# Kernel optimization log

Measured on AMD Instinct MI355X. Metric: run time of the kernel, lower is better.

Reference implementation:

```python
import jax, jax.numpy as jnp
import numpy as np

DIM = 1024
HEADS = 16
HEAD_DIM = DIM // HEADS
LAYERS = 8
HIDDEN = 4 * DIM
VOCAB = 266
MAX_POS = 32768
B = 4
L = 2048
SCALE = HEAD_DIM ** -0.5
EPS = 1e-5


def layer_norm(x, g, b):
    m = jnp.mean(x, axis=-1, keepdims=True)
    v = jnp.mean(jnp.square(x - m), axis=-1, keepdims=True)
    return (x - m) * jax.lax.rsqrt(v + EPS) * g + b


def setup_inputs() -> dict:
    key = jax.random.key(0)
    ks = jax.random.split(key, 16)
    s = 0.02
    return {
        "tokens": jax.random.randint(ks[0], (B, L), 0, VOCAB),
        "tok_emb": jax.random.normal(ks[1], (VOCAB, DIM), jnp.float32) * s,
        "pos_emb": jax.random.normal(ks[2], (MAX_POS, DIM), jnp.float32) * s,
        "ln1_g": jnp.ones((LAYERS, DIM), jnp.float32),
        "ln1_b": jnp.zeros((LAYERS, DIM), jnp.float32),
        "q_w": jax.random.normal(ks[3], (LAYERS, DIM, DIM), jnp.float32) * s,
        "k_w": jax.random.normal(ks[4], (LAYERS, DIM, DIM), jnp.float32) * s,
        "v_w": jax.random.normal(ks[5], (LAYERS, DIM, DIM), jnp.float32) * s,
        "o_w": jax.random.normal(ks[6], (LAYERS, DIM, DIM), jnp.float32) * s,
        "ln2_g": jnp.ones((LAYERS, DIM), jnp.float32),
        "ln2_b": jnp.zeros((LAYERS, DIM), jnp.float32),
        "w1_w": jax.random.normal(ks[7], (LAYERS, HIDDEN, DIM), jnp.float32) * s,
        "wg_w": jax.random.normal(ks[8], (LAYERS, HIDDEN, DIM), jnp.float32) * s,
        "w2_w": jax.random.normal(ks[9], (LAYERS, DIM, HIDDEN), jnp.float32) * s,
        "lnf_g": jnp.ones((DIM,), jnp.float32),
        "lnf_b": jnp.zeros((DIM,), jnp.float32),
        "lm_w": jax.random.normal(ks[10], (VOCAB, DIM), jnp.float32) * s,
    }


def reference(tokens, tok_emb, pos_emb, ln1_g, ln1_b, q_w, k_w, v_w, o_w,
              ln2_g, ln2_b, w1_w, wg_w, w2_w, lnf_g, lnf_b, lm_w):
    Bv, Lv = tokens.shape
    x = tok_emb[tokens] + pos_emb[jnp.arange(Lv)][None, :, :]  # [B,L,D]
    # strictly-upper-triangular causal mask (True = masked)
    rows = jnp.arange(Lv)
    mask = rows[None, :] > rows[:, None]  # [L,L], col > row
    pos_bias = jnp.arange(Lv, dtype=x.dtype) * 0.01  # [L]
    neg_inf = jnp.array(-jnp.inf, dtype=x.dtype)

    for i in range(LAYERS):
        h = layer_norm(x, ln1_g[i], ln1_b[i])
        q = jnp.einsum('bld,ed->ble', h, q_w[i]).reshape(Bv, Lv, HEADS, HEAD_DIM).transpose(0, 2, 1, 3)
        k = jnp.einsum('bld,ed->ble', h, k_w[i]).reshape(Bv, Lv, HEADS, HEAD_DIM).transpose(0, 2, 1, 3)
        v = jnp.einsum('bld,ed->ble', h, v_w[i]).reshape(Bv, Lv, HEADS, HEAD_DIM).transpose(0, 2, 1, 3)
        attn = jnp.einsum('bhqd,bhkd->bhqk', q, k) * SCALE
        attn = jnp.where(mask[None, None, :, :], neg_inf, attn)
        attn = attn + pos_bias[None, None, None, :]
        attn = jax.nn.softmax(attn, axis=-1)
        out = jnp.einsum('bhqk,bhkd->bhqd', attn, v).transpose(0, 2, 1, 3).reshape(Bv, Lv, DIM)
        attn_out = jnp.einsum('bld,ed->ble', out, o_w[i])
        x = x + attn_out
        h2 = layer_norm(x, ln2_g[i], ln2_b[i])
        ff = jnp.einsum('blh,dh->bld', jax.nn.silu(jnp.einsum('bld,hd->blh', h2, w1_w[i])) * jnp.einsum('bld,hd->blh', h2, wg_w[i]), w2_w[i])
        x = x + ff

    last = layer_norm(x[:, -1, :], lnf_g, lnf_b)  # [B, D]
    return jnp.einsum('bd,vd->bv', last, lm_w)  # [B, VOCAB]
```

## Files before the change

kernel.cpp:

```cpp
#include <hip/hip_runtime.h>
#include <hip/hip_bf16.h>
#include <math.h>

#define DIMD 1024
#define HEADS 16
#define HD 64
#define LAYERS 8
#define HIDDEN 4096
#define VOCAB 266
#define NB 4
#define SEQ 2048
#define ROWS (NB*SEQ)
#define LOG2E 1.4426950408889634f
#define QSCALE (0.125f * LOG2E)
#define BIAS2 (0.01f * LOG2E)
#define THR2 8.0f

typedef float f32x4 __attribute__((ext_vector_type(4)));
typedef __bf16 bf16x8 __attribute__((ext_vector_type(8)));
typedef __bf16 bf16x4 __attribute__((ext_vector_type(4)));

__device__ __forceinline__ f32x4 mfma16(bf16x8 a, bf16x8 b, f32x4 c) {
    return __builtin_amdgcn_mfma_f32_16x16x32_bf16(a, b, c, 0, 0, 0);
}

__device__ __forceinline__ void gload16(const __bf16* g, __bf16* l) {
    __builtin_amdgcn_global_load_lds(
        (const __attribute__((address_space(1))) void*)g,
        (__attribute__((address_space(3))) void*)l, 16, 0, 0);
}

__global__ void embed_kernel(const int* __restrict__ tok, const float* __restrict__ te,
                             const float* __restrict__ pe, float* __restrict__ x) {
    int row = blockIdx.x;
    int t = tok[row];
    int l = row & (SEQ - 1);
    int c = threadIdx.x;
    f32x4 tv = *(const f32x4*)(te + (size_t)t * DIMD + c * 4);
    f32x4 pv = *(const f32x4*)(pe + (size_t)l * DIMD + c * 4);
    *(f32x4*)(x + (size_t)row * DIMD + c * 4) = tv + pv;
}

__global__ void cvt_kernel(const float* q, const float* k, const float* v, const float* o,
                           const float* w1, const float* wg, const float* w2,
                           __bf16* __restrict__ dst) {
    const size_t MM = 1024 * 1024;
    const float* src; size_t n; size_t off; int ilv = 0;
    switch (blockIdx.y) {
        case 0: src = q;  n = MM;     off = 0;       break;
        case 1: src = k;  n = MM;     off = MM;      break;
        case 2: src = v;  n = MM;     off = 2 * MM;  break;
        case 3: src = o;  n = MM;     off = 3 * MM;  break;
        case 4: src = w1; n = 4 * MM; off = 4 * MM;  ilv = 1; break;
        case 5: src = wg; n = 4 * MM; off = 4 * MM;  ilv = 2; break;
        default: src = w2; n = 4 * MM; off = 12 * MM; break;
    }
    size_t stride = (size_t)gridDim.x * blockDim.x * 8;
    for (size_t i = ((size_t)blockIdx.x * blockDim.x + threadIdx.x) * 8; i < n; i += stride) {
        f32x4 a = *(const f32x4*)(src + i);
        f32x4 b = *(const f32x4*)(src + i + 4);
        bf16x8 ov;
        ov[0] = (__bf16)a[0]; ov[1] = (__bf16)a[1]; ov[2] = (__bf16)a[2]; ov[3] = (__bf16)a[3];
        ov[4] = (__bf16)b[0]; ov[5] = (__bf16)b[1]; ov[6] = (__bf16)b[2]; ov[7] = (__bf16)b[3];
        size_t di;
        if (ilv) {
            size_t row = i >> 10, col = i & 1023;
            di = off + (((row << 1) | (ilv - 1)) << 10) + col;
        } else {
            di = off + i;
        }
        *(bf16x8*)(dst + di) = ov;
    }
}

template<bool F32OUT>
__global__ void ln_kernel(const float* __restrict__ xin, size_t row_stride,
                          const float* __restrict__ g, const float* __restrict__ bb,
                          void* __restrict__ out) {
    int row = blockIdx.x;
    int c = threadIdx.x;
    const float* xr = xin + (size_t)row * row_stride;
    f32x4 v = *(const f32x4*)(xr + c * 4);
    float s = v[0] + v[1] + v[2] + v[3];
    float s2 = v[0]*v[0] + v[1]*v[1] + v[2]*v[2] + v[3]*v[3];
    #pragma unroll
    for (int o = 32; o; o >>= 1) { s += __shfl_xor(s, o); s2 += __shfl_xor(s2, o); }
    __shared__ float red[8];
    int w = c >> 6, lane = c & 63;
    if (lane == 0) { red[w] = s; red[4 + w] = s2; }
    __syncthreads();
    s = red[0] + red[1] + red[2] + red[3];
    s2 = red[4] + red[5] + red[6] + red[7];
    float mean = s * (1.f / DIMD);
    float var = s2 * (1.f / DIMD) - mean * mean;
    float rstd = rsqrtf(var + 1e-5f);
    f32x4 gv = *(const f32x4*)(g + c * 4);
    f32x4 bv = *(const f32x4*)(bb + c * 4);
    f32x4 o4;
    #pragma unroll
    for (int j = 0; j < 4; ++j) o4[j] = (v[j] - mean) * rstd * gv[j] + bv[j];
    if (F32OUT) {
        *(f32x4*)((float*)out + (size_t)row * DIMD + c * 4) = o4;
    } else {
        bf16x4 hv;
        #pragma unroll
        for (int j = 0; j < 4; ++j) hv[j] = (__bf16)o4[j];
        *(bf16x4*)((__bf16*)out + (size_t)row * DIMD + c * 4) = hv;
    }
}

template<int EPI>
__global__ __launch_bounds__(256, 2)
void gemm_bt(const __bf16* __restrict__ A, const __bf16* __restrict__ W,
             int M, int N, int K,
             __bf16* bdst, float* fdst, float scale) {
    __shared__ __bf16 As[128 * 64];
    __shared__ __bf16 Bs[128 * 64];
    int tid = threadIdx.x;
    int lane = tid & 63, w = tid >> 6;
    int wm = w >> 1, wn = w & 1;
    int g16 = lane >> 4, l16 = lane & 15;
    int m0 = blockIdx.y * 128, n0 = blockIdx.x * 128;
    f32x4 acc[4][4] = {};
    int trow = tid >> 3, tcol = (tid & 7) * 8;
    const __bf16* ga = A + (size_t)(m0 + trow) * K + tcol;
    const __bf16* gb = W + (size_t)(n0 + trow) * K + tcol;

    for (int k0 = 0; k0 < K; k0 += 64) {
        #pragma unroll
        for (int p = 0; p < 4; ++p) {
            gload16(ga + (size_t)(p * 32) * K + k0, As + (p * 256 + w * 64) * 8);
            gload16(gb + (size_t)(p * 32) * K + k0, Bs + (p * 256 + w * 64) * 8);
        }
        __syncthreads();
        #pragma unroll
        for (int kk = 0; kk < 2; ++kk) {
            bf16x8 af[4], bfv[4];
            #pragma unroll
            for (int f = 0; f < 4; ++f) {
                af[f]  = *(const bf16x8*)(As + (wm * 64 + f * 16 + l16) * 64 + kk * 32 + g16 * 8);
                bfv[f] = *(const bf16x8*)(Bs + (wn * 64 + f * 16 + l16) * 64 + kk * 32 + g16 * 8);
            }
            #pragma unroll
            for (int fm = 0; fm < 4; ++fm)
                #pragma unroll
                for (int fn = 0; fn < 4; ++fn)
                    acc[fm][fn] = mfma16(af[fm], bfv[fn], acc[fm][fn]);
        }
        __syncthreads();
    }

    #pragma unroll
    for (int fm = 0; fm < 4; ++fm) {
        int rbase = m0 + wm * 64 + fm * 16 + g16 * 4;
        #pragma unroll
        for (int fn = 0; fn < 4; ++fn) {
            int col = n0 + wn * 64 + fn * 16 + l16;
            if (EPI == 2) {
                #pragma unroll
                for (int j = 0; j < 4; ++j) {
                    size_t idx = (size_t)(rbase + j) * N + col;
                    fdst[idx] += acc[fm][fn][j];
                }
            } else if (EPI == 5) {
                int which = col >> 10;
                int c = col & 1023;
                int hh = c >> 6, d = c & 63;
                if (which == 2) {
                    int b = rbase >> 11, l = rbase & 2047;
                    __bf16* vp = bdst + 2 * (size_t)ROWS * DIMD;
                    bf16x4 hv;
                    #pragma unroll
                    for (int j = 0; j < 4; ++j) hv[j] = (__bf16)acc[fm][fn][j];
                    *(bf16x4*)(vp + ((size_t)(b * HEADS + hh) * HD + d) * SEQ + l) = hv;
                } else {
                    float sc = (which == 0) ? scale : 1.f;
                    __bf16* base = bdst + (size_t)which * ROWS * DIMD;
                    #pragma unroll
                    for (int j = 0; j < 4; ++j) {
                        int row = rbase + j;
                        int b = row >> 11, l = row & 2047;
                        base[(((size_t)(b * HEADS + hh) * SEQ + l) << 6) + d] =
                            (__bf16)(acc[fm][fn][j] * sc);
                    }
                }
            } else if (EPI == 6) {
                #pragma unroll
                for (int j = 0; j < 4; ++j) {
                    float own = acc[fm][fn][j];
                    float other = __shfl_xor(own, 1);
                    if (!(l16 & 1)) {
                        float si = own / (1.f + __expf(-own));
                        bdst[(size_t)(rbase + j) * (N >> 1) + (col >> 1)] = (__bf16)(si * other);
                    }
                }
            }
        }
    }
}

__global__ __launch_bounds__(256, 2)
void attn_kernel(const __bf16* __restrict__ qt, const __bf16* __restrict__ kt,
                 const __bf16* __restrict__ vt, __bf16* __restrict__ ao) {
    int lin = blockIdx.x;
    int bxm = lin >> 6;
    int g = lin & 63;
    int hh = g & 15, b = g >> 4;
    int tid = threadIdx.x, lane = tid & 63, w = tid >> 6;
    int g16 = lane >> 4, l16 = lane & 15;

    __shared__ __bf16 Ks[2][64 * 64];
    __shared__ __bf16 Vs[2][64 * 64];
    __shared__ __bf16 Ps[4 * 32 * 72];
    __bf16* Pw = Ps + w * (32 * 72);

    const __bf16* qbase = qt + (size_t)(b * HEADS + hh) * SEQ * HD;
    const __bf16* kbase = kt + (size_t)(b * HEADS + hh) * SEQ * HD;
    const __bf16* vbase = vt + (size_t)(b * HEADS + hh) * HD * SEQ;

    int rr = lane >> 3;
    int cs8 = ((lane & 7) ^ rr) * 8;

    for (int s = 0; s < 2; ++s) {
        int qtile = (s == 0) ? (15 - bxm) : bxm;
        int qb = qtile * 128;
        int nt = (qb >> 6) + 2;

        bf16x8 qf[2][2];
        #pragma unroll
        for (int rb = 0; rb < 2; ++rb)
            #pragma unroll
            for (int kk = 0; kk < 2; ++kk)
                qf[rb][kk] = *(const bf16x8*)(qbase + (size_t)(qb + w * 32 + rb * 16 + l16) * HD + kk * 32 + g16 * 8);

        f32x4 accO[2][4] = {};
        float mrow[2][4], lrow[2][4];
        #pragma unroll
        for (int rb = 0; rb < 2; ++rb)
            #pragma unroll
            for (int j = 0; j < 4; ++j) { mrow[rb][j] = -1e30f; lrow[rb][j] = 0.f; }

        #pragma unroll
        for (int p = 0; p < 2; ++p) {
            int rbse = p * 32 + w * 8;
            gload16(kbase + (size_t)(rbse + rr) * HD + cs8, Ks[0] + rbse * 64);
            gload16(vbase + (size_t)(rbse + rr) * SEQ + cs8, Vs[0] + rbse * 64);
        }
        __syncthreads();

        for (int t = 0; t < nt; ++t) {
            int cur = t & 1;
            int kv0 = t << 6;

            if (t + 1 < nt) {
                int kv1 = kv0 + 64;
                #pragma unroll
                for (int p = 0; p < 2; ++p) {
                    int rbse = p * 32 + w * 8;
                    gload16(kbase + (size_t)(kv1 + rbse + rr) * HD + cs8, Ks[cur ^ 1] + rbse * 64);
                    gload16(vbase + (size_t)(rbse + rr) * SEQ + kv1 + cs8, Vs[cur ^ 1] + rbse * 64);
                }
            }

            f32x4 sacc[2][4] = {};
            #pragma unroll
            for (int kk = 0; kk < 2; ++kk) {
                bf16x8 kf[4];
                #pragma unroll
                for (int nk = 0; nk < 4; ++nk) {
                    int key = nk * 16 + l16;
                    int bo = (key * 128 + (kk * 32 + g16 * 8) * 2) ^ ((key & 7) << 4);
                    kf[nk] = *(const bf16x8*)((const char*)Ks[cur] + bo);
                }
                #pragma unroll
                for (int rb = 0; rb < 2; ++rb)
                    #pragma unroll
                    for (int nk = 0; nk < 4; ++nk)
                        sacc[rb][nk] = mfma16(qf[rb][kk], kf[nk], sacc[rb][nk]);
            }

            float mx8[2][4];
            #pragma unroll
            for (int rb = 0; rb < 2; ++rb) {
                #pragma unroll
                for (int j = 0; j < 4; ++j) {
                    int qrow = qb + w * 32 + rb * 16 + g16 * 4 + j;
                    float mx = -1e30f;
                    #pragma unroll
                    for (int nk = 0; nk < 4; ++nk) {
                        int key = kv0 + nk * 16 + l16;
                        float sc = sacc[rb][nk][j];
                        sc = (key <= qrow) ? (sc + BIAS2 * (float)key) : -1e30f;
                        sacc[rb][nk][j] = sc;
                        mx = fmaxf(mx, sc);
                    }
                    mx = fmaxf(mx, __shfl_xor(mx, 1));
                    mx = fmaxf(mx, __shfl_xor(mx, 2));
                    mx = fmaxf(mx, __shfl_xor(mx, 4));
                    mx = fmaxf(mx, __shfl_xor(mx, 8));
                    mx8[rb][j] = mx;
                }
            }

            bool ok = true;
            #pragma unroll
            for (int rb = 0; rb < 2; ++rb)
                #pragma unroll
                for (int j = 0; j < 4; ++j)
                    ok &= (mx8[rb][j] <= mrow[rb][j] + THR2);
            if (!__all(ok)) {
                #pragma unroll
                for (int rb = 0; rb < 2; ++rb) {
                    #pragma unroll
                    for (int j = 0; j < 4; ++j) {
                        float mnew = fmaxf(mrow[rb][j], mx8[rb][j]);
                        float rs = exp2f(mrow[rb][j] - mnew);
                        mrow[rb][j] = mnew;
                        lrow[rb][j] *= rs;
                        #pragma unroll
                        for (int nd = 0; nd < 4; ++nd) accO[rb][nd][j] *= rs;
                    }
                }
            }

            #pragma unroll
            for (int rb = 0; rb < 2; ++rb) {
                #pragma unroll
                for (int j = 0; j < 4; ++j) {
                    float m = mrow[rb][j];
                    float ps = 0.f;
                    #pragma unroll
                    for (int nk = 0; nk < 4; ++nk) {
                        float pp = exp2f(sacc[rb][nk][j] - m);
                        ps += pp;
                        Pw[(rb * 16 + g16 * 4 + j) * 72 + nk * 16 + l16] = (__bf16)pp;
                    }
                    lrow[rb][j] += ps;
                }
            }

            #pragma unroll
            for (int kk = 0; kk < 2; ++kk) {
                bf16x8 pf[2];
                #pragma unroll
                for (int rb = 0; rb < 2; ++rb)
                    pf[rb] = *(const bf16x8*)(Pw + (rb * 16 + l16) * 72 + kk * 32 + g16 * 8);
                #pragma unroll
                for (int nd = 0; nd < 4; ++nd) {
                    int d = nd * 16 + l16;
                    int bo = (d * 128 + (kk * 32 + g16 * 8) * 2) ^ ((d & 7) << 4);
                    bf16x8 vf = *(const bf16x8*)((const char*)Vs[cur] + bo);
                    #pragma unroll
                    for (int rb = 0; rb < 2; ++rb)
                        accO[rb][nd] = mfma16(pf[rb], vf, accO[rb][nd]);
                }
            }
            __syncthreads();
        }

        #pragma unroll
        for (int rb = 0; rb < 2; ++rb) {
            #pragma unroll
            for (int j = 0; j < 4; ++j) {
                float l = lrow[rb][j];
                l += __shfl_xor(l, 1);
                l += __shfl_xor(l, 2);
                l += __shfl_xor(l, 4);
                l += __shfl_xor(l, 8);
                lrow[rb][j] = 1.f / l;
            }
        }
        #pragma unroll
        for (int rb = 0; rb < 2; ++rb)
            #pragma unroll
            for (int nd = 0; nd < 4; ++nd)
                #pragma unroll
                for (int j = 0; j < 4; ++j) {
                    int row = qb + w * 32 + rb * 16 + g16 * 4 + j;
                    float o = accO[rb][nd][j] * lrow[rb][j];
                    ao[(size_t)(b * SEQ + row) * DIMD + hh * HD + nd * 16 + l16] = (__bf16)o;
                }
    }
}

__global__ void lm_head(const float* __restrict__ last, const float* __restrict__ lw,
                        float* __restrict__ out) {
    int v = blockIdx.x;
    int c = threadIdx.x, lane = c & 63, w = c >> 6;
    f32x4 wv = *(const f32x4*)(lw + (size_t)v * DIMD + c * 4);
    float a[NB];
    #pragma unroll
    for (int b = 0; b < NB; ++b) {
        f32x4 xv = *(const f32x4*)(last + b * DIMD + c * 4);
        a[b] = wv[0]*xv[0] + wv[1]*xv[1] + wv[2]*xv[2] + wv[3]*xv[3];
    }
    #pragma unroll
    for (int o = 32; o; o >>= 1)
        #pragma unroll
        for (int b = 0; b < NB; ++b) a[b] += __shfl_xor(a[b], o);
    __shared__ float red[4][NB];
    if (lane == 0)
        #pragma unroll
        for (int b = 0; b < NB; ++b) red[w][b] = a[b];
    __syncthreads();
    if (c < NB) {
        float s = red[0][c] + red[1][c] + red[2][c] + red[3][c];
        out[c * VOCAB + v] = s;
    }
}

extern "C" void kernel_launch(void* const* d_in, const int* in_sizes, int n_in,
                              void* d_out, int out_size, void* d_ws, size_t ws_size,
                              hipStream_t stream) {
    const int*   tokens  = (const int*)d_in[0];
    const float* tok_emb = (const float*)d_in[1];
    const float* pos_emb = (const float*)d_in[2];
    const float* ln1_g   = (const float*)d_in[3];
    const float* ln1_b   = (const float*)d_in[4];
    const float* q_w     = (const float*)d_in[5];
    const float* k_w     = (const float*)d_in[6];
    const float* v_w     = (const float*)d_in[7];
    const float* o_w     = (const float*)d_in[8];
    const float* ln2_g   = (const float*)d_in[9];
    const float* ln2_b   = (const float*)d_in[10];
    const float* w1_w    = (const float*)d_in[11];
    const float* wg_w    = (const float*)d_in[12];
    const float* w2_w    = (const float*)d_in[13];
    const float* lnf_g   = (const float*)d_in[14];
    const float* lnf_b   = (const float*)d_in[15];
    const float* lm_w    = (const float*)d_in[16];

    const size_t MM = 1024 * 1024;
    char* p = (char*)d_ws;
    __bf16* wbf = (__bf16*)p;          p += 16 * MM * 2;
    float*  x   = (float*)p;           p += (size_t)ROWS * DIMD * 4;
    __bf16* h   = (__bf16*)p;          p += (size_t)ROWS * DIMD * 2;
    __bf16* qt  = (__bf16*)p;          p += (size_t)ROWS * DIMD * 2;
    __bf16* kt  = (__bf16*)p;          p += (size_t)ROWS * DIMD * 2;
    __bf16* vt  = (__bf16*)p;          p += (size_t)ROWS * DIMD * 2;
    __bf16* ao  = (__bf16*)p;          p += (size_t)ROWS * DIMD * 2;
    __bf16* abuf= (__bf16*)p;          p += (size_t)ROWS * HIDDEN * 2;
    float*  last= (float*)p;           p += NB * DIMD * 4;

    embed_kernel<<<ROWS, 256, 0, stream>>>(tokens, tok_emb, pos_emb, x);

    for (int i = 0; i < LAYERS; ++i) {
        cvt_kernel<<<dim3(256, 7), 256, 0, stream>>>(
            q_w + (size_t)i * MM, k_w + (size_t)i * MM, v_w + (size_t)i * MM, o_w + (size_t)i * MM,
            w1_w + (size_t)i * 4 * MM, wg_w + (size_t)i * 4 * MM, w2_w + (size_t)i * 4 * MM, wbf);
        __bf16* wqkv = wbf;
        __bf16* wo   = wbf + 3 * MM;
        __bf16* w1g  = wbf + 4 * MM;
        __bf16* w2   = wbf + 12 * MM;

        ln_kernel<false><<<ROWS, 256, 0, stream>>>(x, DIMD, ln1_g + i * DIMD, ln1_b + i * DIMD, h);

        gemm_bt<5><<<dim3(24, 64), 256, 0, stream>>>(h, wqkv, ROWS, 3 * DIMD, DIMD, qt, nullptr, QSCALE);

        attn_kernel<<<512, 256, 0, stream>>>(qt, kt, vt, ao);

        gemm_bt<2><<<dim3(8, 64), 256, 0, stream>>>(ao, wo, ROWS, DIMD, DIMD, nullptr, x, 1.f);

        ln_kernel<false><<<ROWS, 256, 0, stream>>>(x, DIMD, ln2_g + i * DIMD, ln2_b + i * DIMD, h);

        gemm_bt<6><<<dim3(64, 64), 256, 0, stream>>>(h, w1g, ROWS, 2 * HIDDEN, DIMD, abuf, nullptr, 1.f);
        gemm_bt<2><<<dim3(8, 64), 256, 0, stream>>>(abuf, w2, ROWS, DIMD, HIDDEN, nullptr, x, 1.f);
    }

    ln_kernel<true><<<NB, 256, 0, stream>>>(x + (size_t)(SEQ - 1) * DIMD, (size_t)SEQ * DIMD,
                                            lnf_g, lnf_b, last);
    lm_head<<<VOCAB, 256, 0, stream>>>(last, lm_w, (float*)d_out);
}
```

Before: 4.256 ms.

## Add double-buffered 256x256 GEMM for QKV and FFN-up, swizzle LDS, raise MFMA priority

Adds a new gemm_big kernel with 256x256 tiles, 512 threads, double-buffered LDS staging with explicit waitcnt and barrier control, and s_setprio around the MFMA bursts. It replaces the QKV and gated-FFN projections, aiming to raise operand reuse and overlap global loads with compute. Both GEMMs now use an XOR swizzle on LDS to avoid bank conflicts, and the attention kernel raises wave priority during its MFMA sections. The large tiles use 128 KB of LDS per block, which limits occupancy. The hand-placed waitcnt is also fragile if the load count changes.

```diff
diff --git a/kernel.cpp b/kernel.cpp
--- a/kernel.cpp
+++ b/kernel.cpp
@@ -122,9 +122,11 @@
     int g16 = lane >> 4, l16 = lane & 15;
     int m0 = blockIdx.y * 128, n0 = blockIdx.x * 128;
     f32x4 acc[4][4] = {};
-    int trow = tid >> 3, tcol = (tid & 7) * 8;
-    const __bf16* ga = A + (size_t)(m0 + trow) * K + tcol;
-    const __bf16* gb = W + (size_t)(n0 + trow) * K + tcol;
+    int trow = tid >> 3;
+    int cs8 = ((tid & 7) ^ (trow & 7)) * 8;
+    const __bf16* ga = A + (size_t)(m0 + trow) * K + cs8;
+    const __bf16* gb = W + (size_t)(n0 + trow) * K + cs8;
+    int xsw = (l16 & 7) << 4;
 
     for (int k0 = 0; k0 < K; k0 += 64) {
         #pragma unroll
@@ -138,8 +140,10 @@
             bf16x8 af[4], bfv[4];
             #pragma unroll
             for (int f = 0; f < 4; ++f) {
-                af[f]  = *(const bf16x8*)(As + (wm * 64 + f * 16 + l16) * 64 + kk * 32 + g16 * 8);
-                bfv[f] = *(const bf16x8*)(Bs + (wn * 64 + f * 16 + l16) * 64 + kk * 32 + g16 * 8);
+                int ar = wm * 64 + f * 16 + l16;
+                int br = wn * 64 + f * 16 + l16;
+                af[f]  = *(const bf16x8*)((const char*)As + ((ar * 128 + kk * 64 + g16 * 16) ^ xsw));
+                bfv[f] = *(const bf16x8*)((const char*)Bs + ((br * 128 + kk * 64 + g16 * 16) ^ xsw));
             }
             #pragma unroll
             for (int fm = 0; fm < 4; ++fm)
@@ -162,7 +166,95 @@
                     size_t idx = (size_t)(rbase + j) * N + col;
                     fdst[idx] += acc[fm][fn][j];
                 }
-            } else if (EPI == 5) {
+            }
+        }
+    }
+}
+
+template<int EPI>
+__global__ __launch_bounds__(512, 2)
+void gemm_big(const __bf16* __restrict__ A, const __bf16* __restrict__ W,
+              int M, int N, int K, __bf16* __restrict__ bdst, float scale) {
+    __shared__ __bf16 As[2][256 * 64];
+    __shared__ __bf16 Bs[2][256 * 64];
+    int tid = threadIdx.x;
+    int lane = tid & 63, wid = tid >> 6;
+    int wm = wid >> 2, wn = wid & 3;
+    int g16 = lane >> 4, l16 = lane & 15;
+    int m0 = blockIdx.y * 256, n0 = blockIdx.x * 256;
+
+    int sr = tid >> 3;
+    int cs8 = ((tid & 7) ^ (sr & 7)) * 8;
+    const __bf16* ga = A + (size_t)(m0 + sr) * K + cs8;
+    const __bf16* gb = W + (size_t)(n0 + sr) * K + cs8;
+
+    auto stage = [&](int buf, int kof) {
+        #pragma unroll
+        for (int p = 0; p < 4; ++p) {
+            gload16(ga + (size_t)(p * 64) * K + kof, As[buf] + (p * 64 + sr) * 64 + (tid & 7) * 8);
+            gload16(gb + (size_t)(p * 64) * K + kof, Bs[buf] + (p * 64 + sr) * 64 + (tid & 7) * 8);
+        }
+    };
+
+    f32x4 acc[8][4] = {};
+    int NT = K >> 6;
+    stage(0, 0);
+    stage(1, 64);
+    int xsw = (l16 & 7) << 4;
+
+    for (int t = 0; t < NT; ++t) {
+        int cur = t & 1;
+        if (t + 1 < NT) asm volatile("s_waitcnt vmcnt(8)" ::: "memory");
+        else            asm volatile("s_waitcnt vmcnt(0)" ::: "memory");
+        __builtin_amdgcn_s_barrier();
+        __builtin_amdgcn_sched_barrier(0);
+        const char* Ab = (const char*)As[cur];
+        const char* Bb = (const char*)Bs[cur];
+        bf16x8 bfr[4][2];
+        #pragma unroll
+        for (int q = 0; q < 4; ++q) {
+            bf16x8 afr[2][2];
+            #pragma unroll
+            for (int dm = 0; dm < 2; ++dm)
+                #pragma unroll
+                for (int kk = 0; kk < 2; ++kk) {
+                    int row = wm * 128 + (q * 2 + dm) * 16 + l16;
+                    afr[dm][kk] = *(const bf16x8*)(Ab + ((row * 128 + kk * 64 + g16 * 16) ^ xsw));
+                }
+            if (q == 0) {
+                #pragma unroll
+                for (int n = 0; n < 4; ++n)
+                    #pragma unroll
+                    for (int kk = 0; kk < 2; ++kk) {
+                        int row = wn * 64 + n * 16 + l16;
+                        bfr[n][kk] = *(const bf16x8*)(Bb + ((row * 128 + kk * 64 + g16 * 16) ^ xsw));
+                    }
+            }
+            asm volatile("s_waitcnt lgkmcnt(0)" ::: "memory");
+            __builtin_amdgcn_sched_barrier(0);
+            __builtin_amdgcn_s_setprio(1);
+            #pragma unroll
+            for (int dm = 0; dm < 2; ++dm)
+                #pragma unroll
+                for (int n = 0; n < 4; ++n)
+                    #pragma unroll
+                    for (int kk = 0; kk < 2; ++kk)
+                        acc[q * 2 + dm][n] = mfma16(afr[dm][kk], bfr[n][kk], acc[q * 2 + dm][n]);
+            __builtin_amdgcn_s_setprio(0);
+            __builtin_amdgcn_sched_barrier(0);
+        }
+        asm volatile("s_waitcnt lgkmcnt(0)" ::: "memory");
+        __builtin_amdgcn_s_barrier();
+        if (t + 2 < NT) stage(cur, (t + 2) << 6);
+    }
+
+    #pragma unroll
+    for (int m = 0; m < 8; ++m) {
+        int rbase = m0 + wm * 128 + m * 16 + g16 * 4;
+        #pragma unroll
+        for (int n = 0; n < 4; ++n) {
+            int col = n0 + wn * 64 + n * 16 + l16;
+            if (EPI == 5) {
                 int which = col >> 10;
                 int c = col & 1023;
                 int hh = c >> 6, d = c & 63;
@@ -171,7 +263,7 @@
                     __bf16* vp = bdst + 2 * (size_t)ROWS * DIMD;
                     bf16x4 hv;
                     #pragma unroll
-                    for (int j = 0; j < 4; ++j) hv[j] = (__bf16)acc[fm][fn][j];
+                    for (int j = 0; j < 4; ++j) hv[j] = (__bf16)acc[m][n][j];
                     *(bf16x4*)(vp + ((size_t)(b * HEADS + hh) * HD + d) * SEQ + l) = hv;
                 } else {
                     float sc = (which == 0) ? scale : 1.f;
@@ -181,13 +273,13 @@
                         int row = rbase + j;
                         int b = row >> 11, l = row & 2047;
                         base[(((size_t)(b * HEADS + hh) * SEQ + l) << 6) + d] =
-                            (__bf16)(acc[fm][fn][j] * sc);
+                            (__bf16)(acc[m][n][j] * sc);
                     }
                 }
             } else if (EPI == 6) {
                 #pragma unroll
                 for (int j = 0; j < 4; ++j) {
-                    float own = acc[fm][fn][j];
+                    float own = acc[m][n][j];
                     float other = __shfl_xor(own, 1);
                     if (!(l16 & 1)) {
                         float si = own / (1.f + __expf(-own));
@@ -263,6 +355,7 @@
             }
 
             f32x4 sacc[2][4] = {};
+            __builtin_amdgcn_s_setprio(1);
             #pragma unroll
             for (int kk = 0; kk < 2; ++kk) {
                 bf16x8 kf[4];
@@ -278,6 +371,7 @@
                     for (int nk = 0; nk < 4; ++nk)
                         sacc[rb][nk] = mfma16(qf[rb][kk], kf[nk], sacc[rb][nk]);
             }
+            __builtin_amdgcn_s_setprio(0);
 
             float mx8[2][4];
             #pragma unroll
@@ -339,6 +433,7 @@
                 }
             }
 
+            __builtin_amdgcn_s_setprio(1);
             #pragma unroll
             for (int kk = 0; kk < 2; ++kk) {
                 bf16x8 pf[2];
@@ -355,6 +450,7 @@
                         accO[rb][nd] = mfma16(pf[rb], vf, accO[rb][nd]);
                 }
             }
+            __builtin_amdgcn_s_setprio(0);
             __syncthreads();
         }
 
@@ -455,7 +551,7 @@
 
         ln_kernel<false><<<ROWS, 256, 0, stream>>>(x, DIMD, ln1_g + i * DIMD, ln1_b + i * DIMD, h);
 
-        gemm_bt<5><<<dim3(24, 64), 256, 0, stream>>>(h, wqkv, ROWS, 3 * DIMD, DIMD, qt, nullptr, QSCALE);
+        gemm_big<5><<<dim3(12, 32), 512, 0, stream>>>(h, wqkv, ROWS, 3 * DIMD, DIMD, qt, QSCALE);
 
         attn_kernel<<<512, 256, 0, stream>>>(qt, kt, vt, ao);
 
@@ -463,7 +559,8 @@
 
         ln_kernel<false><<<ROWS, 256, 0, stream>>>(x, DIMD, ln2_g + i * DIMD, ln2_b + i * DIMD, h);
 
-        gemm_bt<6><<<dim3(64, 64), 256, 0, stream>>>(h, w1g, ROWS, 2 * HIDDEN, DIMD, abuf, nullptr, 1.f);
+        gemm_big<6><<<dim3(32, 32), 512, 0, stream>>>(h, w1g, ROWS, 2 * HIDDEN, DIMD, abuf, 1.f);
+
         gemm_bt<2><<<dim3(8, 64), 256, 0, stream>>>(abuf, w2, ROWS, DIMD, HIDDEN, nullptr, x, 1.f);
     }
 
```

New measurement: 4.312 ms. No clear change (+1.3%).
